# Kernel optimization log

Measured on AMD Instinct MI355X. Metric: run time of the kernel, lower is better.

## Reference

```python
import jax, jax.numpy as jnp
import numpy as np

B, T, D, H = 4, 4096, 1024, 16
CAP = 0.5


def setup_inputs() -> dict:
    key = jax.random.key(0)
    ks = jax.random.split(key, 8)
    s = 0.02
    n = lambda k, shape: jax.random.normal(k, shape, dtype=jnp.float32) * s
    return {
        "x": jax.random.normal(ks[0], (B, T, D), dtype=jnp.float32),
        "w_router": n(ks[1], (D,)),
        "in_proj_w": n(ks[2], (3 * D, D)),
        "in_proj_b": jnp.zeros((3 * D,), jnp.float32),
        "out_proj_w": n(ks[3], (D, D)),
        "out_proj_b": jnp.zeros((D,), jnp.float32),
        "w1": n(ks[4], (4 * D, D)),
        "b1": jnp.zeros((4 * D,), jnp.float32),
        "w2": n(ks[5], (D, 4 * D)),
        "b2": jnp.zeros((D,), jnp.float32),
        "ln1_g": jnp.ones((D,), jnp.float32),
        "ln1_b": jnp.zeros((D,), jnp.float32),
        "ln2_g": jnp.ones((D,), jnp.float32),
        "ln2_b": jnp.zeros((D,), jnp.float32),
    }


def _ln(x, g, b, eps=1e-5):
    mu = jnp.mean(x, -1, keepdims=True)
    var = jnp.var(x, -1, keepdims=True)  # population variance, matches torch LayerNorm
    return (x - mu) * jax.lax.rsqrt(var + eps) * g + b


def reference(x, w_router, in_proj_w, in_proj_b, out_proj_w, out_proj_b,
              w1, b1, w2, b2, ln1_g, ln1_b, ln2_g, ln2_b):
    Bx, Tx, Dx = x.shape
    k = max(1, int(Tx * CAP))  # tokens routed through the block, same k for every batch row
    logits = x @ w_router  # (B,T) scalar router scores
    aux = jnp.mean(logits ** 2) * 0.01
    # top-k selection; sort indices ascending = boolean-mask gather order in torch
    idx = jnp.sort(jax.lax.top_k(logits, k)[1], axis=-1)  # (B,k)
    xs = jnp.take_along_axis(x, idx[:, :, None], axis=1)  # (B,k,D)

    h = _ln(xs, ln1_g, ln1_b)
    qkv = h @ in_proj_w.T + in_proj_b  # (B,k,3D)
    q, kk, v = jnp.split(qkv, 3, axis=-1)
    dh = Dx // H
    heads = lambda t: t.reshape(Bx, k, H, dh).transpose(0, 2, 1, 3)  # (B,H,k,dh)
    q, kk, v = heads(q), heads(kk), heads(v)
    scores = jnp.einsum('bhqd,bhkd->bhqk', q, kk) / jnp.sqrt(jnp.float32(dh))
    attn = jax.nn.softmax(scores, axis=-1)
    o = jnp.einsum('bhqk,bhkd->bhqd', attn, v).transpose(0, 2, 1, 3).reshape(Bx, k, Dx)
    o = o @ out_proj_w.T + out_proj_b
    xs = xs + o
    h2 = _ln(xs, ln2_g, ln2_b)
    ff = jax.nn.gelu(h2 @ w1.T + b1, approximate=False) @ w2.T + b2
    xs = xs + ff
    # scatter processed tokens back; unselected tokens pass through unchanged
    out = x.at[jnp.arange(Bx)[:, None], idx].set(xs)
    return out, aux
```

## Files before the change

kernel.cpp:

```cpp
#include <hip/hip_runtime.h>

#define B_    4
#define T_    4096
#define D_    1024
#define H_    16
#define DH_   64
#define KTOK  2048
#define MROWS (B_*KTOK)

typedef unsigned short u16;
typedef __attribute__((ext_vector_type(8))) short short8;
typedef __attribute__((ext_vector_type(4))) float f32x4;
typedef __attribute__((ext_vector_type(4))) unsigned int u32x4;
typedef __attribute__((ext_vector_type(2))) unsigned int u32x2;
typedef __attribute__((ext_vector_type(4))) unsigned short u16x4;

static __device__ __forceinline__ u16 f2bf(float f) {
  union { float f; unsigned int u; } a; a.f = f;
  unsigned int u = a.u;
  unsigned int r = (u + 0x7FFFu + ((u >> 16) & 1u)) >> 16;
  return (u16)r;
}

#if defined(__has_builtin)
#if __has_builtin(__builtin_amdgcn_exp2f)
#define EXP2F(x) __builtin_amdgcn_exp2f(x)
#endif
#endif
#ifndef EXP2F
#define EXP2F(x) exp2f(x)
#endif

static __device__ __forceinline__ float gelu_f(float v) {
  float x = fabsf(v) * 0.70710678118654752f;
  float t = __builtin_amdgcn_rcpf(1.0f + 0.3275911f * x);
  float p = t * (0.254829592f + t * (-0.284496736f + t * (1.421413741f +
            t * (-1.453152027f + t * 1.061405429f))));
  float e = EXP2F(-1.4426950408889634f * x * x);
  float er = 1.0f - p * e;
  er = (v < 0.0f) ? -er : er;
  return 0.5f * v * (1.0f + er);
}

static __device__ __forceinline__ unsigned int pkbf_t(float a, float b) {
  unsigned int ua = __builtin_bit_cast(unsigned int, a);
  unsigned int ub = __builtin_bit_cast(unsigned int, b);
  return __builtin_amdgcn_perm(ub, ua, 0x07060302u);
}

static __device__ __forceinline__ void gld_lds16(const u16* g, u16* l) {
  __builtin_amdgcn_global_load_lds((__attribute__((address_space(1))) void*)g,
                                   (__attribute__((address_space(3))) void*)l, 16, 0, 0);
}

#define WAITV(N) asm volatile("s_waitcnt vmcnt(" #N ")" ::: "memory")

__global__ void __launch_bounds__(256) router_kernel(const float* __restrict__ x,
    const float* __restrict__ wr, float* __restrict__ logits, float* __restrict__ auxacc)
{
  int tid = threadIdx.x; int lane = tid & 63, wave = tid >> 6;
  int row = blockIdx.x * 4 + wave;
  const float* xr = x + (size_t)row * D_;
  float dot = 0.f;
#pragma unroll
  for (int j = 0; j < 4; j++) {
    int c = j * 256 + lane * 4;
    f32x4 xv = *(const f32x4*)(xr + c);
    f32x4 wv = *(const f32x4*)(wr + c);
    dot += xv[0]*wv[0] + xv[1]*wv[1] + xv[2]*wv[2] + xv[3]*wv[3];
  }
#pragma unroll
  for (int d = 1; d < 64; d <<= 1) dot += __shfl_xor(dot, d);
  __shared__ float red[4];
  if (lane == 0) { logits[row] = dot; red[wave] = dot; }
  __syncthreads();
  if (tid == 0) {
    float a = red[0]*red[0] + red[1]*red[1] + red[2]*red[2] + red[3]*red[3];
    atomicAdd(auxacc, a);
  }
}

__global__ void __launch_bounds__(256) rankp_kernel(const float* __restrict__ logits,
    int* __restrict__ rnk)
{
  __shared__ float ll[256];
  const int b = blockIdx.y, ch = blockIdx.z;
  const int tid = threadIdx.x;
  const float* lg = logits + (size_t)b * T_;
  const int j0 = ch * 256;
  ll[tid] = lg[j0 + tid];
  __syncthreads();
  const int t = blockIdx.x * 256 + tid;
  const float my = lg[t];
  int rank = 0;
#pragma unroll 4
  for (int j = 0; j < 256; j += 4) {
    f32x4 lj = *(const f32x4*)&ll[j];
    int jg = j0 + j;
    rank += (lj[0] > my) || (lj[0] == my && (jg+0) < t);
    rank += (lj[1] > my) || (lj[1] == my && (jg+1) < t);
    rank += (lj[2] > my) || (lj[2] == my && (jg+2) < t);
    rank += (lj[3] > my) || (lj[3] == my && (jg+3) < t);
  }
  atomicAdd(&rnk[(size_t)b * T_ + t], rank);
}

__global__ void __launch_bounds__(256) lnpass_kernel(const float* __restrict__ x,
    const int* __restrict__ rnk, const float* __restrict__ g, const float* __restrict__ bb,
    float* __restrict__ xs_out, u16* __restrict__ hout, float* __restrict__ out,
    int* __restrict__ idx, const float* __restrict__ acc, float* __restrict__ auxout)
{
  int row = blockIdx.x;
  int tid = threadIdx.x;
  if (row == 0 && tid == 0) auxout[0] = acc[0] * (0.01f / (float)(B_ * T_));
  const float* srow = x + (size_t)row * D_;
  f32x4 v = *(const f32x4*)(srow + tid * 4);
  int r = rnk[row];
  if (r >= KTOK) {
    *(f32x4*)(out + (size_t)row * D_ + tid * 4) = v;
    return;
  }
  if (tid == 0) idx[(row >> 12) * KTOK + r] = row & (T_ - 1);
  size_t mrow = (size_t)(row >> 12) * KTOK + r;
  float s  = v[0] + v[1] + v[2] + v[3];
  float sq = v[0]*v[0] + v[1]*v[1] + v[2]*v[2] + v[3]*v[3];
#pragma unroll
  for (int d = 1; d < 64; d <<= 1) { s += __shfl_xor(s, d); sq += __shfl_xor(sq, d); }
  __shared__ float rs[4], rq[4];
  int lane = tid & 63, wave = tid >> 6;
  if (lane == 0) { rs[wave] = s; rq[wave] = sq; }
  __syncthreads();
  s  = rs[0] + rs[1] + rs[2] + rs[3];
  sq = rq[0] + rq[1] + rq[2] + rq[3];
  float mean = s * (1.0f / D_);
  float var  = sq * (1.0f / D_) - mean * mean;
  float rstd = rsqrtf(var + 1e-5f);
  f32x4 gg = *(const f32x4*)(g + tid * 4);
  f32x4 bv = *(const f32x4*)(bb + tid * 4);
  *(f32x4*)(xs_out + mrow * D_ + tid * 4) = v;
  u16x4 o;
#pragma unroll
  for (int j = 0; j < 4; j++) o[j] = f2bf((v[j] - mean) * rstd * gg[j] + bv[j]);
  *(u16x4*)(hout + mrow * D_ + tid * 4) = o;
}

__global__ void __launch_bounds__(256) ln2_kernel(const float* __restrict__ src,
    const float* __restrict__ g, const float* __restrict__ bb, u16* __restrict__ hout)
{
  int row = blockIdx.x;
  int tid = threadIdx.x;
  const float* srow = src + (size_t)row * D_;
  f32x4 v = *(const f32x4*)(srow + tid * 4);
  float s  = v[0] + v[1] + v[2] + v[3];
  float sq = v[0]*v[0] + v[1]*v[1] + v[2]*v[2] + v[3]*v[3];
#pragma unroll
  for (int d = 1; d < 64; d <<= 1) { s += __shfl_xor(s, d); sq += __shfl_xor(sq, d); }
  __shared__ float rs[4], rq[4];
  int lane = tid & 63, wave = tid >> 6;
  if (lane == 0) { rs[wave] = s; rq[wave] = sq; }
  __syncthreads();
  s  = rs[0] + rs[1] + rs[2] + rs[3];
  sq = rq[0] + rq[1] + rq[2] + rq[3];
  float mean = s * (1.0f / D_);
  float var  = sq * (1.0f / D_) - mean * mean;
  float rstd = rsqrtf(var + 1e-5f);
  f32x4 gg = *(const f32x4*)(g + tid * 4);
  f32x4 bv = *(const f32x4*)(bb + tid * 4);
  u16x4 o;
#pragma unroll
  for (int j = 0; j < 4; j++) o[j] = f2bf((v[j] - mean) * rstd * gg[j] + bv[j]);
  *(u16x4*)(hout + (size_t)row * D_ + tid * 4) = o;
}

__global__ void __launch_bounds__(256) f2bf_all(const float* __restrict__ s0, const float* __restrict__ s1,
    const float* __restrict__ s2, const float* __restrict__ s3,
    u16* __restrict__ d0, u16* __restrict__ d1, u16* __restrict__ d2, u16* __restrict__ d3)
{
  const size_t c0 = (size_t)3 * D_ * D_, c1 = (size_t)4 * D_ * D_, c2 = (size_t)8 * D_ * D_;
  size_t e = (size_t)blockIdx.x * 1024 + (size_t)threadIdx.x * 4;
  const float* s; u16* d; size_t off;
  if (e < c0)      { s = s0; d = d0; off = e; }
  else if (e < c1) { s = s1; d = d1; off = e - c0; }
  else if (e < c2) { s = s2; d = d2; off = e - c1; }
  else             { s = s3; d = d3; off = e - c2; }
  f32x4 v = *(const f32x4*)(s + off);
  u16x4 o; o[0]=f2bf(v[0]); o[1]=f2bf(v[1]); o[2]=f2bf(v[2]); o[3]=f2bf(v[3]);
  *(u16x4*)(d + off) = o;
}

template<int EPI>
__global__ void __launch_bounds__(256, 2) gemm_bt(
    const u16* __restrict__ A, const u16* __restrict__ W,
    const float* __restrict__ bias, float* __restrict__ xs,
    u16* __restrict__ Cb, float* __restrict__ outf,
    const int* __restrict__ idx, u16* __restrict__ vtb, int M, int N, int K)
{
  __shared__ u16 As[2][128 * 64];
  __shared__ u16 Ws[2][128 * 64];
  const int tid = threadIdx.x;
  const int lane = tid & 63, wave = tid >> 6;
  const int m16 = lane & 15, quad = (lane >> 4) & 3;

  const int gx = gridDim.x;
  const int id = blockIdx.y * gx + blockIdx.x;
  const int cpx = (gx * (int)gridDim.y) >> 3;
  const int tl = (id & 7) * cpx + (id >> 3);
  const int bx = tl % gx, by = tl / gx;

  const size_t arow0 = (size_t)by * 128;
  const size_t wrow0 = (size_t)bx * 128;

  const int trow = tid >> 3;
  const int tcc  = (tid ^ trow) & 7;
  auto stagepc = [&](const u16* g0, u16* l0) {
    gld_lds16(g0 + (size_t)trow * K + tcc * 8,        l0 + (size_t)(tid & ~63) * 8);
    gld_lds16(g0 + (size_t)(32 + trow) * K + tcc * 8, l0 + 2048 + (size_t)(tid & ~63) * 8);
  };
  auto stage_tile = [&](int u, int s) {
    size_t kn = (size_t)u * 64;
    stagepc(A + (arow0)      * K + kn, &As[s][0]);
    stagepc(A + (arow0 + 64) * K + kn, &As[s][64 * 64]);
    stagepc(W + (wrow0)      * K + kn, &Ws[s][0]);
    stagepc(W + (wrow0 + 64) * K + kn, &Ws[s][64 * 64]);
  };

  auto ldA = [&](short8 (&f)[2][2], const u16* h) {
#pragma unroll
    for (int mt = 0; mt < 2; mt++) {
      int rr = wave * 32 + mt * 16 + m16;
      int sw = rr & 7;
#pragma unroll
      for (int kk = 0; kk < 2; kk++)
        f[mt][kk] = *(const short8*)&h[rr * 64 + (((kk * 4 + quad) ^ sw) * 8)];
    }
  };
  auto ldB = [&](short8 (&f)[4][2], const u16* h, int half) {
#pragma unroll
    for (int nt = 0; nt < 4; nt++) {
      int rb = half * 64 + nt * 16 + m16;
      int sw = rb & 7;
#pragma unroll
      for (int kk = 0; kk < 2; kk++)
        f[nt][kk] = *(const short8*)&h[rb * 64 + (((kk * 4 + quad) ^ sw) * 8)];
    }
  };

  f32x4 acc[2][8];
#pragma unroll
  for (int mt = 0; mt < 2; mt++)
#pragma unroll
    for (int n = 0; n < 8; n++) acc[mt][n] = (f32x4)0.0f;

  stage_tile(0, 0);

  const int NT = K >> 6;
  short8 af[2][2], bf[4][2], bf2[4][2];

  for (int t = 0; t < NT; t++) {
    const int cur = t & 1;
    const bool last = (t == NT - 1);

    WAITV(2);
    __builtin_amdgcn_s_barrier();
    __builtin_amdgcn_sched_barrier(0);
    if (!last) stage_tile(t + 1, cur ^ 1);

    ldA(af, &As[cur][0]);
    ldB(bf, &Ws[cur][0], 0);
    __builtin_amdgcn_s_setprio(1);
#pragma unroll
    for (int mt = 0; mt < 2; mt++)
#pragma unroll
      for (int nt = 0; nt < 4; nt++)
#pragma unroll
        for (int kk = 0; kk < 2; kk++)
          acc[mt][nt] = __builtin_amdgcn_mfma_f32_16x16x32_bf16(af[mt][kk], bf[nt][kk], acc[mt][nt], 0, 0, 0);
    __builtin_amdgcn_s_setprio(0);

    if (last) { WAITV(0); } else { WAITV(8); }
    __builtin_amdgcn_s_barrier();
    __builtin_amdgcn_sched_barrier(0);

    ldB(bf2, &Ws[cur][0], 1);
    __builtin_amdgcn_s_setprio(1);
#pragma unroll
    for (int mt = 0; mt < 2; mt++)
#pragma unroll
      for (int nt = 0; nt < 4; nt++)
#pragma unroll
        for (int kk = 0; kk < 2; kk++)
          acc[mt][4 + nt] = __builtin_amdgcn_mfma_f32_16x16x32_bf16(af[mt][kk], bf2[nt][kk], acc[mt][4 + nt], 0, 0, 0);
    __builtin_amdgcn_s_setprio(0);
  }

#pragma unroll
  for (int half = 0; half < 2; half++) {
#pragma unroll
    for (int mt = 0; mt < 2; mt++) {
#pragma unroll
      for (int nt = 0; nt < 4; nt++) {
        f32x4 a = acc[mt][half * 4 + nt];
        size_t col = wrow0 + half * 64 + nt * 16 + m16;
        float bvv = bias[col];
        size_t rowb = arow0 + wave * 32 + mt * 16 + quad * 4;
        if (EPI == 0) {
          if ((int)col < 2 * D_) {
            float sc = ((int)col < D_) ? 0.18033688f : 1.0f;
#pragma unroll
            for (int r = 0; r < 4; r++)
              Cb[(rowb + r) * (size_t)N + col] = f2bf((a[r] + bvv) * sc);
          } else {
            int hdh = (int)col - 2 * D_;
            int bb2 = (int)(rowb >> 11);
            int tok = (int)(rowb & (KTOK - 1));
            u16x4 o;
#pragma unroll
            for (int r = 0; r < 4; r++) o[r] = f2bf(a[r] + bvv);
            *(u16x4*)&vtb[(((size_t)(bb2 * H_) + (hdh >> 6)) * 64 + (hdh & 63)) * KTOK + tok] = o;
          }
        } else if (EPI == 1) {
#pragma unroll
          for (int r = 0; r < 4; r++) {
            size_t o = (rowb + r) * (size_t)N + col;
            xs[o] = xs[o] + (a[r] + bvv);
          }
        } else {
#pragma unroll
          for (int r = 0; r < 4; r++) {
            size_t row = rowb + r;
            int b = (int)(row >> 11);
            int i = (int)(row & (KTOK - 1));
            int t = idx[b * KTOK + i];
            float vv = xs[row * (size_t)D_ + col] + (a[r] + bvv);
            outf[((size_t)b * T_ + t) * D_ + col] = vv;
          }
        }
      }
    }
  }
}

__global__ void __launch_bounds__(512, 1) gemm_ff1(
    const u16* __restrict__ A, const u16* __restrict__ W,
    const float* __restrict__ bias, u16* __restrict__ Cb, int M, int N, int K)
{
  __shared__ u16 Asm[2][2][128 * 64];
  __shared__ u16 Bsm[2][2][128 * 64];

  const int tid = threadIdx.x;
  const int lane = tid & 63;
  const int w = tid >> 6;
  const int m16 = lane & 15, quad = (lane >> 4) & 3;
  const int rowA = (w >> 2) * 64;
  const int rowB = (w & 3) * 32;

  const int gx = gridDim.x;
  const int id = blockIdx.y * gx + blockIdx.x;
  const int cpx = (gx * (int)gridDim.y) >> 3;
  const int tl = (id & 7) * cpx + (id >> 3);
  const int bx = tl % gx, by = tl / gx;

  const int arow0 = by * 256;
  const int wcol0 = bx * 256;

  const int th8 = tid >> 3;
  const int ccs = (tid ^ th8) & 7;
  auto stage = [&](const u16* g0, u16* l0) {
    gld_lds16(g0 + (size_t)th8 * K + ccs * 8,        l0 + (size_t)(tid & ~63) * 8);
    gld_lds16(g0 + (size_t)(64 + th8) * K + ccs * 8, l0 + 4096 + (size_t)(tid & ~63) * 8);
  };
  auto stage_tile = [&](int u, int s) {
    size_t kn = (size_t)u * 64;
    stage(A + (size_t)arow0 * K + kn,         &Asm[s][0][0]);
    stage(W + (size_t)wcol0 * K + kn,         &Bsm[s][0][0]);
    stage(A + (size_t)(arow0 + 128) * K + kn, &Asm[s][1][0]);
    stage(W + (size_t)(wcol0 + 128) * K + kn, &Bsm[s][1][0]);
  };

  auto ldA = [&](short8 (&f)[4][2], const u16* h) {
#pragma unroll
    for (int mt = 0; mt < 4; mt++) {
      int rr = rowA + mt * 16 + m16;
      int sw = rr & 7;
#pragma unroll
      for (int kk = 0; kk < 2; kk++)
        f[mt][kk] = *(const short8*)&h[rr * 64 + (((kk * 4 + quad) ^ sw) * 8)];
    }
  };
  auto ldB = [&](short8 (&f)[2][2], const u16* h) {
#pragma unroll
    for (int nt = 0; nt < 2; nt++) {
      int rb = rowB + nt * 16 + m16;
      int sw = rb & 7;
#pragma unroll
      for (int kk = 0; kk < 2; kk++)
        f[nt][kk] = *(const short8*)&h[rb * 64 + (((kk * 4 + quad) ^ sw) * 8)];
    }
  };

  f32x4 acc[4][4][2];
#pragma unroll
  for (int q = 0; q < 4; q++)
#pragma unroll
    for (int mt = 0; mt < 4; mt++)
#pragma unroll
      for (int nt = 0; nt < 2; nt++) acc[q][mt][nt] = (f32x4)0.0f;

#define MMQ(QD, FA, FB) do { \
  __builtin_amdgcn_s_setprio(1); \
  _Pragma("unroll") for (int mt = 0; mt < 4; mt++) \
  _Pragma("unroll") for (int nt = 0; nt < 2; nt++) \
  _Pragma("unroll") for (int kk = 0; kk < 2; kk++) \
    acc[QD][mt][nt] = __builtin_amdgcn_mfma_f32_16x16x32_bf16(FA[mt][kk], FB[nt][kk], acc[QD][mt][nt], 0, 0, 0); \
  __builtin_amdgcn_s_setprio(0); } while (0)

  stage_tile(0, 0);

  const int NT = K >> 6;
  short8 af[4][2], af2[4][2], bf[2][2], bf2[2][2];

  for (int t = 0; t < NT; t++) {
    const int cur = t & 1;
    const bool last = (t == NT - 1);

    WAITV(4);
    __builtin_amdgcn_s_barrier();
    __builtin_amdgcn_sched_barrier(0);
    if (!last) stage_tile(t + 1, cur ^ 1);

    ldA(af, &Asm[cur][0][0]);
    ldB(bf, &Bsm[cur][0][0]);
    MMQ(0, af, bf);

    if (last) { WAITV(0); } else { WAITV(8); }
    __builtin_amdgcn_s_barrier();
    __builtin_amdgcn_sched_barrier(0);

    ldB(bf2, &Bsm[cur][1][0]);
    MMQ(1, af, bf2);
    ldA(af2, &Asm[cur][1][0]);
    MMQ(2, af2, bf);
    MMQ(3, af2, bf2);
  }
#undef MMQ

#pragma unroll
  for (int qd = 0; qd < 4; qd++) {
    const int ha = qd >> 1, hb = qd & 1;
#pragma unroll
    for (int mt = 0; mt < 4; mt++) {
#pragma unroll
      for (int nt = 0; nt < 2; nt++) {
        f32x4 a = acc[qd][mt][nt];
        size_t col = (size_t)wcol0 + hb * 128 + (w & 3) * 32 + nt * 16 + m16;
        float bvv = bias[col];
        size_t rowb = (size_t)arow0 + ha * 128 + (w >> 2) * 64 + mt * 16 + quad * 4;
#pragma unroll
        for (int r = 0; r < 4; r++)
          Cb[(rowb + r) * (size_t)N + col] = f2bf(gelu_f(a[r] + bvv));
      }
    }
  }
}

__global__ void __launch_bounds__(512, 4) attn_kernel(const u16* __restrict__ qkv,
                                                      const u16* __restrict__ vtb,
                                                      u16* __restrict__ obuf)
{
  __shared__ u16 Ks[2][64 * 64];
  __shared__ u16 Vs[2][64 * 64];
  __shared__ u16 Ps[8][2][16 * 64];

  const int tid = threadIdx.x;
  const int lane = tid & 63, wave = tid >> 6;
  const int m16 = lane & 15, quad = lane >> 4;
  const int bh = blockIdx.x;
  const int b = bh >> 4, h = bh & 15;
  const int q0 = blockIdx.y * 256 + wave * 32;

  const u16* base = qkv + ((size_t)b * KTOK) * (3 * D_) + h * DH_;
  const u16* vb   = vtb + (size_t)bh * 64 * KTOK;

  short8 qf[2][2];
#pragma unroll
  for (int qh = 0; qh < 2; qh++) {
    const u16* qrow = base + (size_t)(q0 + qh * 16 + m16) * (3 * D_);
    qf[qh][0] = *(const short8*)(qrow + quad * 8);
    qf[qh][1] = *(const short8*)(qrow + 32 + quad * 8);
  }
  short8 vone;
#pragma unroll
  for (int i = 0; i < 8; i++) vone[i] = (short)0x3F80;

  f32x4 oacc[2][4];
#pragma unroll
  for (int qh = 0; qh < 2; qh++)
#pragma unroll
    for (int nt = 0; nt < 4; nt++) oacc[qh][nt] = (f32x4)0.0f;
  f32x4 lacc[2] = {(f32x4)0.0f, (f32x4)0.0f};

  auto stage_tile = [&](const u16* g0, size_t rstride, u16* lds) {
    int key = tid >> 3;
    int cc = (tid ^ key) & 7;
    gld_lds16(g0 + (size_t)key * rstride + cc * 8, lds + (size_t)(tid & ~63) * 8);
  };

  stage_tile(base + D_, 3 * D_, &Ks[0][0]);
  stage_tile(vb, KTOK, &Vs[0][0]);
  __syncthreads();

  const int sw = m16 & 7;
  int buf = 0;
  for (int tk = 0; tk < KTOK; tk += 64) {
    if (tk + 64 < KTOK) {
      stage_tile(base + (size_t)(tk + 64) * (3 * D_) + D_, 3 * D_, &Ks[buf ^ 1][0]);
      stage_tile(vb + (tk + 64), KTOK, &Vs[buf ^ 1][0]);
    }
    const u16* Kb = &Ks[buf][0];
    const u16* Vb = &Vs[buf][0];

    f32x4 sacc[2][4];
#pragma unroll
    for (int qh = 0; qh < 2; qh++)
#pragma unroll
      for (int nt = 0; nt < 4; nt++) sacc[qh][nt] = (f32x4)0.0f;
    __builtin_amdgcn_s_setprio(1);
#pragma unroll
    for (int nt = 0; nt < 4; nt++) {
      int row = nt * 16 + m16;
      int ksw = row & 7;
      short8 kf0 = *(const short8*)&Kb[row * 64 + ((quad ^ ksw) * 8)];
      short8 kf1 = *(const short8*)&Kb[row * 64 + (((4 + quad) ^ ksw) * 8)];
#pragma unroll
      for (int qh = 0; qh < 2; qh++) {
        sacc[qh][nt] = __builtin_amdgcn_mfma_f32_16x16x32_bf16(kf0, qf[qh][0], sacc[qh][nt], 0, 0, 0);
        sacc[qh][nt] = __builtin_amdgcn_mfma_f32_16x16x32_bf16(kf1, qf[qh][1], sacc[qh][nt], 0, 0, 0);
      }
    }
    __builtin_amdgcn_s_setprio(0);

    short8 vf[4][2];
#pragma unroll
    for (int nt = 0; nt < 4; nt++) {
      int row = nt * 16 + m16;
      int vsw = row & 7;
      vf[nt][0] = *(const short8*)&Vb[row * 64 + ((quad ^ vsw) * 8)];
      vf[nt][1] = *(const short8*)&Vb[row * 64 + (((4 + quad) ^ vsw) * 8)];
    }

#pragma unroll
    for (int qh = 0; qh < 2; qh++) {
#pragma unroll
      for (int nt = 0; nt < 4; nt++) {
        f32x4 p;
#pragma unroll
        for (int r = 0; r < 4; r++) p[r] = EXP2F(sacc[qh][nt][r]);
        u32x2 w2; w2[0] = pkbf_t(p[0], p[1]); w2[1] = pkbf_t(p[2], p[3]);
        int c16 = 2 * nt + (quad >> 1);
        *(u32x2*)&Ps[wave][qh][m16 * 64 + ((c16 ^ sw) * 8) + (quad & 1) * 4] = w2;
      }
    }
    short8 pa[2][2];
#pragma unroll
    for (int qh = 0; qh < 2; qh++) {
      pa[qh][0] = *(const short8*)&Ps[wave][qh][m16 * 64 + ((quad ^ sw) * 8)];
      pa[qh][1] = *(const short8*)&Ps[wave][qh][m16 * 64 + (((4 + quad) ^ sw) * 8)];
    }
    __builtin_amdgcn_s_setprio(1);
#pragma unroll
    for (int qh = 0; qh < 2; qh++) {
#pragma unroll
      for (int nt = 0; nt < 4; nt++) {
        oacc[qh][nt] = __builtin_amdgcn_mfma_f32_16x16x32_bf16(pa[qh][0], vf[nt][0], oacc[qh][nt], 0, 0, 0);
        oacc[qh][nt] = __builtin_amdgcn_mfma_f32_16x16x32_bf16(pa[qh][1], vf[nt][1], oacc[qh][nt], 0, 0, 0);
      }
      lacc[qh] = __builtin_amdgcn_mfma_f32_16x16x32_bf16(pa[qh][0], vone, lacc[qh], 0, 0, 0);
      lacc[qh] = __builtin_amdgcn_mfma_f32_16x16x32_bf16(pa[qh][1], vone, lacc[qh], 0, 0, 0);
    }
    __builtin_amdgcn_s_setprio(0);

    __syncthreads();
    buf ^= 1;
  }

#pragma unroll
  for (int qh = 0; qh < 2; qh++) {
    f32x4 rl;
#pragma unroll
    for (int r = 0; r < 4; r++) rl[r] = 1.0f / lacc[qh][r];
#pragma unroll
    for (int nt = 0; nt < 4; nt++)
#pragma unroll
      for (int r = 0; r < 4; r++) {
        int qq = q0 + qh * 16 + quad * 4 + r;
        float v = oacc[qh][nt][r] * rl[r];
        obuf[((size_t)b * KTOK + qq) * D_ + h * DH_ + nt * 16 + m16] = f2bf(v);
      }
  }
}

extern "C" void kernel_launch(void* const* d_in, const int* in_sizes, int n_in,
                              void* d_out, int out_size, void* d_ws, size_t ws_size,
                              hipStream_t stream)
{
  (void)in_sizes; (void)n_in; (void)out_size; (void)ws_size;
  const float* x          = (const float*)d_in[0];
  const float* w_router   = (const float*)d_in[1];
  const float* in_proj_w  = (const float*)d_in[2];
  const float* in_proj_b  = (const float*)d_in[3];
  const float* out_proj_w = (const float*)d_in[4];
  const float* out_proj_b = (const float*)d_in[5];
  const float* w1         = (const float*)d_in[6];
  const float* b1         = (const float*)d_in[7];
  const float* w2         = (const float*)d_in[8];
  const float* b2         = (const float*)d_in[9];
  const float* ln1g       = (const float*)d_in[10];
  const float* ln1b       = (const float*)d_in[11];
  const float* ln2g       = (const float*)d_in[12];
  const float* ln2b       = (const float*)d_in[13];
  float* out = (float*)d_out;

  char* w = (char*)d_ws;
  auto alloc = [&](size_t bytes) -> char* {
    char* p = w; w += (bytes + 255) & ~(size_t)255; return p;
  };
  float* logits = (float*)alloc((size_t)B_ * T_ * 4);
  int*   rnk    = (int*)  alloc((size_t)B_ * T_ * 4);
  int*   idx    = (int*)  alloc((size_t)B_ * KTOK * 4);
  float* auxacc = (float*)alloc(256);
  u16* inpw  = (u16*)alloc((size_t)3 * D_ * D_ * 2);
  u16* outpw = (u16*)alloc((size_t)D_ * D_ * 2);
  u16* w1b   = (u16*)alloc((size_t)4 * D_ * D_ * 2);
  u16* w2b   = (u16*)alloc((size_t)4 * D_ * D_ * 2);
  float* xs  = (float*)alloc((size_t)MROWS * D_ * 4);
  u16* hbuf  = (u16*)alloc((size_t)MROWS * D_ * 2);
  char* region = alloc((size_t)MROWS * 4 * D_ * 2);
  u16* qkvb = (u16*)region;
  u16* obuf = (u16*)(region + (size_t)MROWS * 3 * D_ * 2);
  u16* ffb  = (u16*)region;
  u16* vtb  = (u16*)alloc((size_t)B_ * H_ * DH_ * KTOK * 2);

  (void)hipMemsetAsync(auxacc, 0, 4, stream);
  (void)hipMemsetAsync(rnk, 0, (size_t)B_ * T_ * 4, stream);

  router_kernel<<<B_ * T_ / 4, 256, 0, stream>>>(x, w_router, logits, auxacc);
  rankp_kernel<<<dim3(T_ / 256, B_, 16), 256, 0, stream>>>(logits, rnk);
  lnpass_kernel<<<B_ * T_, 256, 0, stream>>>(x, rnk, ln1g, ln1b, xs, hbuf, out,
                                             idx, auxacc, out + (size_t)B_ * T_ * D_);

  f2bf_all<<<12 * D_ * D_ / 1024, 256, 0, stream>>>(in_proj_w, out_proj_w, w1, w2,
                                                    inpw, outpw, w1b, w2b);

  gemm_bt<0><<<dim3(3 * D_ / 128, MROWS / 128), 256, 0, stream>>>(
      hbuf, inpw, in_proj_b, nullptr, qkvb, nullptr, nullptr, vtb, MROWS, 3 * D_, D_);
  attn_kernel<<<dim3(B_ * H_, KTOK / 256), 512, 0, stream>>>(qkvb, vtb, obuf);
  gemm_bt<1><<<dim3(D_ / 128, MROWS / 128), 256, 0, stream>>>(
      obuf, outpw, out_proj_b, xs, nullptr, nullptr, nullptr, nullptr, MROWS, D_, D_);
  ln2_kernel<<<MROWS, 256, 0, stream>>>(xs, ln2g, ln2b, hbuf);
  gemm_ff1<<<dim3(4 * D_ / 256, MROWS / 256), 512, 0, stream>>>(
      hbuf, w1b, b1, ffb, MROWS, 4 * D_, D_);
  gemm_bt<3><<<dim3(D_ / 128, MROWS / 128), 256, 0, stream>>>(
      ffb, w2b, b2, xs, nullptr, out, idx, nullptr, MROWS, D_, 4 * D_);
}
```

Before: 639.4 us.

## Triple-buffer attention K/V loads and write head-major output for out-projection

The attention kernel moves from double to triple buffering of its K/V tiles. It now waits on vmcnt plus a bare barrier instead of a full __syncthreads, so tile t+2 can be in flight while tile t is computed. Occupancy is declared as 2 blocks per CU instead of 4. Attention output is also written head-major as (b,h,token,dh), contiguous per head, and the out-projection GEMM gets a template mode that reads A tiles from that layout. This changes the store pattern and the GEMM A-load addressing. It assumes that 128-row tiles never cross a batch boundary and that each 64-wide K chunk maps to exactly one head.

```diff
diff --git a/kernel.cpp b/kernel.cpp
--- a/kernel.cpp
+++ b/kernel.cpp
@@ -188,7 +188,7 @@
   *(u16x4*)(d + off) = o;
 }
 
-template<int EPI>
+template<int EPI, bool AHM = false>
 __global__ void __launch_bounds__(256, 2) gemm_bt(
     const u16* __restrict__ A, const u16* __restrict__ W,
     const float* __restrict__ bias, float* __restrict__ xs,
@@ -212,16 +212,23 @@
 
   const int trow = tid >> 3;
   const int tcc  = (tid ^ trow) & 7;
-  auto stagepc = [&](const u16* g0, u16* l0) {
-    gld_lds16(g0 + (size_t)trow * K + tcc * 8,        l0 + (size_t)(tid & ~63) * 8);
-    gld_lds16(g0 + (size_t)(32 + trow) * K + tcc * 8, l0 + 2048 + (size_t)(tid & ~63) * 8);
+  auto stagepc = [&](const u16* g0, size_t rs, u16* l0) {
+    gld_lds16(g0 + (size_t)trow * rs + tcc * 8,        l0 + (size_t)(tid & ~63) * 8);
+    gld_lds16(g0 + (size_t)(32 + trow) * rs + tcc * 8, l0 + 2048 + (size_t)(tid & ~63) * 8);
   };
   auto stage_tile = [&](int u, int s) {
     size_t kn = (size_t)u * 64;
-    stagepc(A + (arow0)      * K + kn, &As[s][0]);
-    stagepc(A + (arow0 + 64) * K + kn, &As[s][64 * 64]);
-    stagepc(W + (wrow0)      * K + kn, &Ws[s][0]);
-    stagepc(W + (wrow0 + 64) * K + kn, &Ws[s][64 * 64]);
+    if (AHM) {
+      const u16* Ab = A + (arow0 >> 11) * (size_t)(H_ * KTOK * DH_)
+                        + (arow0 & (KTOK - 1)) * DH_ + (size_t)u * (KTOK * DH_);
+      stagepc(Ab,            64, &As[s][0]);
+      stagepc(Ab + 64 * 64,  64, &As[s][64 * 64]);
+    } else {
+      stagepc(A + (arow0)      * K + kn, K, &As[s][0]);
+      stagepc(A + (arow0 + 64) * K + kn, K, &As[s][64 * 64]);
+    }
+    stagepc(W + (wrow0)      * K + kn, K, &Ws[s][0]);
+    stagepc(W + (wrow0 + 64) * K + kn, K, &Ws[s][64 * 64]);
   };
 
   auto ldA = [&](short8 (&f)[2][2], const u16* h) {
@@ -463,12 +470,12 @@
   }
 }
 
-__global__ void __launch_bounds__(512, 4) attn_kernel(const u16* __restrict__ qkv,
+__global__ void __launch_bounds__(512, 2) attn_kernel(const u16* __restrict__ qkv,
                                                       const u16* __restrict__ vtb,
                                                       u16* __restrict__ obuf)
 {
-  __shared__ u16 Ks[2][64 * 64];
-  __shared__ u16 Vs[2][64 * 64];
+  __shared__ u16 Ks[3][64 * 64];
+  __shared__ u16 Vs[3][64 * 64];
   __shared__ u16 Ps[8][2][16 * 64];
 
   const int tid = threadIdx.x;
@@ -499,22 +506,28 @@
     for (int nt = 0; nt < 4; nt++) oacc[qh][nt] = (f32x4)0.0f;
   f32x4 lacc[2] = {(f32x4)0.0f, (f32x4)0.0f};
 
-  auto stage_tile = [&](const u16* g0, size_t rstride, u16* lds) {
+  auto stage_kv = [&](int u, int s) {
     int key = tid >> 3;
     int cc = (tid ^ key) & 7;
-    gld_lds16(g0 + (size_t)key * rstride + cc * 8, lds + (size_t)(tid & ~63) * 8);
-  };
-
-  stage_tile(base + D_, 3 * D_, &Ks[0][0]);
-  stage_tile(vb, KTOK, &Vs[0][0]);
-  __syncthreads();
+    gld_lds16(base + (size_t)(u * 64 + key) * (3 * D_) + D_ + cc * 8,
+              &Ks[s][0] + (size_t)(tid & ~63) * 8);
+    gld_lds16(vb + (u * 64) + (size_t)key * KTOK + cc * 8,
+              &Vs[s][0] + (size_t)(tid & ~63) * 8);
+  };
+
+  const int NT = KTOK / 64;
+  stage_kv(0, 0);
+  stage_kv(1, 1);
+  WAITV(2);
+  __builtin_amdgcn_s_barrier();
+  __builtin_amdgcn_sched_barrier(0);
 
   const int sw = m16 & 7;
   int buf = 0;
-  for (int tk = 0; tk < KTOK; tk += 64) {
-    if (tk + 64 < KTOK) {
-      stage_tile(base + (size_t)(tk + 64) * (3 * D_) + D_, 3 * D_, &Ks[buf ^ 1][0]);
-      stage_tile(vb + (tk + 64), KTOK, &Vs[buf ^ 1][0]);
+  for (int t = 0; t < NT; t++) {
+    if (t + 2 < NT) {
+      int s2 = buf + 2; if (s2 >= 3) s2 -= 3;
+      stage_kv(t + 2, s2);
     }
     const u16* Kb = &Ks[buf][0];
     const u16* Vb = &Vs[buf][0];
@@ -579,8 +592,12 @@
     }
     __builtin_amdgcn_s_setprio(0);
 
-    __syncthreads();
-    buf ^= 1;
+    if (t < NT - 1) {
+      if (t < NT - 2) { WAITV(2); } else { WAITV(0); }
+      __builtin_amdgcn_s_barrier();
+      __builtin_amdgcn_sched_barrier(0);
+    }
+    buf = (buf == 2) ? 0 : buf + 1;
   }
 
 #pragma unroll
@@ -594,7 +611,7 @@
       for (int r = 0; r < 4; r++) {
         int qq = q0 + qh * 16 + quad * 4 + r;
         float v = oacc[qh][nt][r] * rl[r];
-        obuf[((size_t)b * KTOK + qq) * D_ + h * DH_ + nt * 16 + m16] = f2bf(v);
+        obuf[((size_t)bh * KTOK + qq) * DH_ + nt * 16 + m16] = f2bf(v);
       }
   }
 }
@@ -654,7 +671,7 @@
   gemm_bt<0><<<dim3(3 * D_ / 128, MROWS / 128), 256, 0, stream>>>(
       hbuf, inpw, in_proj_b, nullptr, qkvb, nullptr, nullptr, vtb, MROWS, 3 * D_, D_);
   attn_kernel<<<dim3(B_ * H_, KTOK / 256), 512, 0, stream>>>(qkvb, vtb, obuf);
-  gemm_bt<1><<<dim3(D_ / 128, MROWS / 128), 256, 0, stream>>>(
+  gemm_bt<1, true><<<dim3(D_ / 128, MROWS / 128), 256, 0, stream>>>(
       obuf, outpw, out_proj_b, xs, nullptr, nullptr, nullptr, nullptr, MROWS, D_, D_);
   ln2_kernel<<<MROWS, 256, 0, stream>>>(xs, ln2g, ln2b, hbuf);
   gemm_ff1<<<dim3(4 * D_ / 256, MROWS / 256), 512, 0, stream>>>(
```

After: 634.8 us. Within noise of the previous version (-0.7%).
